# Optimization experiments

Hardware: AMD Instinct MI355X
Metric: run time of the kernel (lower is better)

## Reference

```python
import jax, jax.numpy as jnp
import numpy as np
from jax import lax

K = 3
STRIDE = 1
PAD = 1


def setup_inputs() -> dict:
    key = jax.random.key(0)
    k0, k1, k2, k3 = jax.random.split(key, 4)
    B, C, H, W, O = 8, 128, 64, 64, 128
    x = jax.random.normal(k0, (B, C, H, W), jnp.float32)
    # offset_conv: Conv2d(C, 2*K*K) - small init so sampled offsets stay moderate
    w_off = jax.random.normal(k1, (2 * K * K, C, K, K), jnp.float32) * 0.01
    b_off = jnp.zeros((2 * K * K,), jnp.float32)
    # deform_conv main weight, kaiming-ish scale
    w_def = jax.random.normal(k2, (O, C, K, K), jnp.float32) * (1.0 / np.sqrt(C * K * K))
    b_def = jax.random.normal(k3, (O,), jnp.float32) * 0.01
    return {"x": x, "w_off": w_off, "b_off": b_off, "w_def": w_def, "b_def": b_def}


def _conv2d(x, w, b, stride, pad):
    y = lax.conv_general_dilated(
        x, w, window_strides=(stride, stride), padding=[(pad, pad), (pad, pad)],
        dimension_numbers=("NCHW", "OIHW", "NCHW"))
    return y + b[None, :, None, None]


def _bilinear_sample(x, py, px):
    """x: [B,C,Hin,Win]; py,px: [B,KK,H,W] -> [B,C,KK,H,W] with zero padding."""
    B, C, Hin, Win = x.shape
    iy0f = jnp.floor(py)
    ix0f = jnp.floor(px)
    wy = py - iy0f  # grad of floor is 0, so d(wy)/d(py) = 1 (matches deform conv)
    wx = px - ix0f
    iy0 = iy0f.astype(jnp.int32)
    ix0 = ix0f.astype(jnp.int32)

    def gather(iy, ix):
        valid = (iy >= 0) & (iy < Hin) & (ix >= 0) & (ix < Win)
        iyc = jnp.clip(iy, 0, Hin - 1)
        ixc = jnp.clip(ix, 0, Win - 1)
        g = jax.vmap(lambda xb, a, b: xb[:, a, b])(x, iyc, ixc)  # [B,C,KK,H,W]
        return g * valid[:, None].astype(x.dtype)

    v00 = gather(iy0, ix0)
    v01 = gather(iy0, ix0 + 1)
    v10 = gather(iy0 + 1, ix0)
    v11 = gather(iy0 + 1, ix0 + 1)
    wy_ = wy[:, None]
    wx_ = wx[:, None]
    return (v00 * (1 - wy_) * (1 - wx_) + v01 * (1 - wy_) * wx_
            + v10 * wy_ * (1 - wx_) + v11 * wy_ * wx_)


def reference(x, w_off, b_off, w_def, b_def):
    B, C, H, W = x.shape
    O = w_def.shape[0]
    KK = K * K
    # 1) standard conv predicting offsets: [B, 2*KK, Hout, Wout]
    offsets = _conv2d(x, w_off, b_off, STRIDE, PAD)
    Hout, Wout = offsets.shape[2], offsets.shape[3]
    # torchvision layout: interleaved (dy, dx) per kernel tap
    off = offsets.reshape(B, KK, 2, Hout, Wout)
    off_y, off_x = off[:, :, 0], off[:, :, 1]  # [B,KK,Hout,Wout]
    # 2) base sampling grid per kernel tap
    kys, kxs = jnp.meshgrid(jnp.arange(K), jnp.arange(K), indexing="ij")
    kys = kys.reshape(KK).astype(jnp.float32)
    kxs = kxs.reshape(KK).astype(jnp.float32)
    hs = (jnp.arange(Hout) * STRIDE - PAD).astype(jnp.float32)
    ws = (jnp.arange(Wout) * STRIDE - PAD).astype(jnp.float32)
    base_y = hs[None, :, None] + kys[:, None, None]  # [KK,Hout,1]
    base_x = ws[None, None, :] + kxs[:, None, None]  # [KK,1,Wout]
    py = base_y[None] + off_y  # [B,KK,Hout,Wout]
    px = base_x[None] + off_x
    # 3) gather bilinear-sampled patches then dense contraction (im2col GEMM)
    sampled = _bilinear_sample(x, py, px)  # [B,C,KK,Hout,Wout]
    out = jnp.einsum("bckhw,ock->bohw", sampled, w_def.reshape(O, C, KK))
    return out + b_def[None, :, None, None]
```

## Files before the change

kernel.cpp:

```cpp
#include <hip/hip_runtime.h>
#include <hip/hip_bf16.h>

#define BB 8
#define CC 128
#define HH 64
#define WW 64
#define OO 128
#define NJ 18
#define HW 4096

typedef unsigned short u16;
typedef unsigned int u32;
typedef __attribute__((ext_vector_type(8))) __bf16 bf16x8;
typedef __attribute__((ext_vector_type(4))) float f32x4;

__device__ __forceinline__ u16 f2bf(float f) {
    u32 u = __float_as_uint(f);
    u += 0x7fffu + ((u >> 16) & 1u);
    return (u16)(u >> 16);
}
__device__ __forceinline__ float bflo(u32 u) { return __uint_as_float(u << 16); }
__device__ __forceinline__ float bfhi(u32 u) { return __uint_as_float(u & 0xffff0000u); }
__device__ __forceinline__ u32 pk2bf(float s0, float s1) {
    union { __hip_bfloat162 h; u32 u; } cv;
    cv.h = __float22bfloat162_rn(make_float2(s0, s1));
    return cv.u;
}

__global__ __launch_bounds__(256)
void k_xT(const float* __restrict__ x, u16* __restrict__ xT) {
    __shared__ float tile[64][129];
    const int t = threadIdx.x;
    const int b = blockIdx.x >> 6;
    const int hw0 = (blockIdx.x & 63) << 6;
    const float* xb = x + (size_t)b * CC * HW + hw0;
    const int tw = t & 63, tc = t >> 6;
#pragma unroll
    for (int r = 0; r < 32; ++r) {
        int c = r * 4 + tc;
        tile[tw][c] = xb[c * HW + tw];
    }
    __syncthreads();
    u16* dst = xT + ((size_t)b * HW + hw0) * CC;
#pragma unroll
    for (int r = 0; r < 4; ++r) {
        int item = t + (r << 8);
        int seg = item & 15, hw = item >> 4;
        union { u32 d[4]; uint4 v; } p;
#pragma unroll
        for (int i = 0; i < 4; ++i)
            p.d[i] = pk2bf(tile[hw][seg * 8 + 2 * i], tile[hw][seg * 8 + 2 * i + 1]);
        *(uint4*)&dst[hw * CC + seg * 8] = p.v;
    }
}

__global__ void k_prep(const float* __restrict__ w_def,
                       const float* __restrict__ w_off,
                       u16* __restrict__ wT, u16* __restrict__ wA) {
    int idx = blockIdx.x * 256 + threadIdx.x;
    if (idx < 9 * OO * CC) {
        int c = idx & 127, o = (idx >> 7) & 127, kk = idx >> 14;
        wT[idx] = f2bf(w_def[(o * CC + c) * 9 + kk]);
    }
    if (idx < 32 * 1152) {
        int k = idx % 1152, j = idx / 1152;
        int q = k >> 7, c = k & 127;
        wA[idx] = (j < NJ) ? f2bf(w_off[(j * CC + c) * 9 + q]) : (u16)0;
    }
}

__global__ __launch_bounds__(256, 2)
void k_off(const u16* __restrict__ xT, const u16* __restrict__ wA,
           const float* __restrict__ b_off, float* __restrict__ offs) {
    __shared__ u16 s_x[198 * 128];
    const int t = threadIdx.x, lane = t & 63, wv = t >> 6;
    const int posl = lane & 15, kg = lane >> 4;
    const int b = blockIdx.x & 7, h = blockIdx.x >> 3;

    for (int it = t; it < 3168; it += 256) {
        int seg = it & 15, pix = it >> 4;
        int r = pix / 66, wp = pix - r * 66;
        int y = h - 1 + r, w = wp - 1;
        uint4 v = make_uint4(0, 0, 0, 0);
        if (y >= 0 && y < HH && w >= 0 && w < WW)
            v = *(const uint4*)&xT[((size_t)(b * HW) + y * WW + w) * CC + seg * 8];
        *(uint4*)&s_x[pix * 128 + ((seg ^ (pix & 15)) * 8)] = v;
    }
    __syncthreads();

    f32x4 acc0 = {0.f, 0.f, 0.f, 0.f}, acc1 = {0.f, 0.f, 0.f, 0.f};
    for (int q = 0; q < 9; ++q) {
        int qy = q / 3, qx = q - qy * 3;
        int pix = qy * 66 + (wv * 16 + posl) + qx;
        int prow = pix * 128, pxor = pix & 15;
#pragma unroll
        for (int ki = 0; ki < 4; ++ki) {
            int ks = q * 4 + ki;
            int cidx = ki * 4 + kg;
            bf16x8 bfr = *(const bf16x8*)&s_x[prow + ((cidx ^ pxor) * 8)];
            bf16x8 a0 = *(const bf16x8*)&wA[posl * 1152 + ks * 32 + kg * 8];
            bf16x8 a1 = *(const bf16x8*)&wA[(16 + posl) * 1152 + ks * 32 + kg * 8];
            acc0 = __builtin_amdgcn_mfma_f32_16x16x32_bf16(a0, bfr, acc0, 0, 0, 0);
            acc1 = __builtin_amdgcn_mfma_f32_16x16x32_bf16(a1, bfr, acc1, 0, 0, 0);
        }
    }
    const int pos = wv * 16 + posl;
#pragma unroll
    for (int r = 0; r < 4; ++r) {
        int j = kg * 4 + r;
        offs[(b * NJ + j) * HW + h * WW + pos] = acc0[r] + b_off[j];
    }
#pragma unroll
    for (int r = 0; r < 4; ++r) {
        int j = 16 + kg * 4 + r;
        if (j < NJ) offs[(b * NJ + j) * HW + h * WW + pos] = acc1[r] + b_off[j];
    }
}

__global__ __launch_bounds__(256, 2)
void k_main(const u16* __restrict__ xT, const float* __restrict__ offs,
            const u16* __restrict__ wT, const float* __restrict__ b_def,
            float* __restrict__ out) {
    __shared__ u16 s_samp[64 * 128];

    const int t = threadIdx.x, lane = t & 63, wv = t >> 6;
    const int posl = lane & 15, kg = lane >> 4;
    const int b = blockIdx.x & 7;
    const int h = blockIdx.x >> 3;
    const char* xb = (const char*)xT + (size_t)b * (HW * CC * 2);

    const int gpos = t >> 2;
    const int segsub = t & 3;

    f32x4 acc[4][2];
#pragma unroll
    for (int mt = 0; mt < 4; ++mt) {
        acc[mt][0] = (f32x4){0.f, 0.f, 0.f, 0.f};
        acc[mt][1] = (f32x4){0.f, 0.f, 0.f, 0.f};
    }

#pragma unroll 1
    for (int kk = 0; kk < 9; ++kk) {
        int ky = kk / 3, kx = kk - ky * 3;
        float oy = offs[(b * NJ + 2 * kk) * HW + h * WW + gpos];
        float ox = offs[(b * NJ + 2 * kk + 1) * HW + h * WW + gpos];
        float py = (float)(h - 1 + ky) + oy;
        float px = (float)(gpos - 1 + kx) + ox;
        float fy = floorf(py), fx = floorf(px);
        int iy0 = (int)fy, ix0 = (int)fx;
        float wy = py - fy, wx = px - fx;
        int iy1 = iy0 + 1, ix1 = ix0 + 1;
        float my0 = (iy0 >= 0 && iy0 < HH) ? 1.0f : 0.0f;
        float my1 = (iy1 >= 0 && iy1 < HH) ? 1.0f : 0.0f;
        float mx0 = (ix0 >= 0 && ix0 < WW) ? 1.0f : 0.0f;
        float mx1 = (ix1 >= 0 && ix1 < WW) ? 1.0f : 0.0f;
        int iy0c = min(max(iy0, 0), HH - 1), iy1c = min(max(iy1, 0), HH - 1);
        int ix0c = min(max(ix0, 0), WW - 1), ix1c = min(max(ix1, 0), WW - 1);
        float wy1 = 1.0f - wy, wx1 = 1.0f - wx;
        float cwx = my0 * mx0 * wy1 * wx1, cwy = my0 * mx1 * wy1 * wx;
        float cwz = my1 * mx0 * wy * wx1,  cww = my1 * mx1 * wy * wx;
        int cox = (iy0c * WW + ix0c) << 8, coy = (iy0c * WW + ix1c) << 8;
        int coz = (iy1c * WW + ix0c) << 8, cow = (iy1c * WW + ix1c) << 8;

        const int slotbase = gpos * 128;
        const int pxor = gpos & 15;
#pragma unroll
        for (int j = 0; j < 4; ++j) {
            const int seg = segsub + 4 * j;
            const int sb = seg * 16;
            uint4 q00 = *(const uint4*)(xb + cox + sb);
            uint4 q01 = *(const uint4*)(xb + coy + sb);
            uint4 q10 = *(const uint4*)(xb + coz + sb);
            uint4 q11 = *(const uint4*)(xb + cow + sb);
            const u32* u00 = (const u32*)&q00;
            const u32* u01 = (const u32*)&q01;
            const u32* u10 = (const u32*)&q10;
            const u32* u11 = (const u32*)&q11;
            union { u32 d[4]; uint4 v; } p;
#pragma unroll
            for (int i = 0; i < 4; ++i) {
                float s0 = cwx * bflo(u00[i]) + cwy * bflo(u01[i])
                         + cwz * bflo(u10[i]) + cww * bflo(u11[i]);
                float s1 = cwx * bfhi(u00[i]) + cwy * bfhi(u01[i])
                         + cwz * bfhi(u10[i]) + cww * bfhi(u11[i]);
                p.d[i] = pk2bf(s0, s1);
            }
            *(uint4*)&s_samp[slotbase + ((seg ^ pxor) * 8)] = p.v;
        }
        __syncthreads();

        {
            const int o0 = wv * 32;
            const u16* wkk = wT + kk * (OO * CC);
            bf16x8 wfr[4][2];
#pragma unroll
            for (int ct = 0; ct < 4; ++ct) {
#pragma unroll
                for (int nt = 0; nt < 2; ++nt) {
                    int o = o0 + nt * 16 + posl;
                    wfr[ct][nt] = *(const bf16x8*)&wkk[o * CC + ct * 32 + kg * 8];
                }
            }
#pragma unroll
            for (int ct = 0; ct < 4; ++ct) {
                const int chunk = ct * 4 + kg;
#pragma unroll
                for (int mt = 0; mt < 4; ++mt) {
                    bf16x8 afr = *(const bf16x8*)
                        &s_samp[(mt * 16 + posl) * 128 + ((chunk ^ posl) * 8)];
                    acc[mt][0] = __builtin_amdgcn_mfma_f32_16x16x32_bf16(
                        afr, wfr[ct][0], acc[mt][0], 0, 0, 0);
                    acc[mt][1] = __builtin_amdgcn_mfma_f32_16x16x32_bf16(
                        afr, wfr[ct][1], acc[mt][1], 0, 0, 0);
                }
            }
        }
        __syncthreads();
    }

#pragma unroll
    for (int nt = 0; nt < 2; ++nt) {
        const int o = wv * 32 + nt * 16 + posl;
        const float bd = b_def[o];
        float* orow = out + ((b * OO + o) * HH + h) * WW;
#pragma unroll
        for (int mt = 0; mt < 4; ++mt) {
            float4 res;
            res.x = acc[mt][nt][0] + bd;
            res.y = acc[mt][nt][1] + bd;
            res.z = acc[mt][nt][2] + bd;
            res.w = acc[mt][nt][3] + bd;
            *(float4*)&orow[mt * 16 + kg * 4] = res;
        }
    }
}

extern "C" void kernel_launch(void* const* d_in, const int* in_sizes, int n_in,
                              void* d_out, int out_size, void* d_ws, size_t ws_size,
                              hipStream_t stream) {
    const float* x     = (const float*)d_in[0];
    const float* w_off = (const float*)d_in[1];
    const float* b_off = (const float*)d_in[2];
    const float* w_def = (const float*)d_in[3];
    const float* b_def = (const float*)d_in[4];
    float* out = (float*)d_out;

    float* offs = (float*)d_ws;
    u16*   xT   = (u16*)(offs + BB * NJ * HW);
    u16*   wT   = xT + (size_t)BB * HW * CC;
    u16*   wA   = wT + 9 * OO * CC;

    k_xT  <<<512, 256, 0, stream>>>(x, xT);
    k_prep<<<576, 256, 0, stream>>>(w_def, w_off, wT, wA);
    k_off <<<512, 256, 0, stream>>>(xT, wA, b_off, offs);
    k_main<<<512, 256, 0, stream>>>(xT, offs, wT, b_def, out);
}
```

Measured before the change: 139.5 us.

## Double-buffer sampled tile and prefetch next tap's gather during MFMA

Splits the shared sample buffer into two halves and software-pipelines the kernel-tap loop. The next tap's offsets and bilinear gather loads are issued before the current tap's MFMA work, then interpolated into the alternate buffer afterwards, which drops one barrier per iteration. The goal is to hide global gather latency behind the matrix math. In exchange it holds 16 uint4 registers of prefetched data across the MFMA section and doubles LDS use to 32KB, which may lower occupancy under launch_bounds(256,2) or cause spills.

```diff
diff --git a/kernel.cpp b/kernel.cpp
--- a/kernel.cpp
+++ b/kernel.cpp
@@ -121,7 +121,7 @@
 void k_main(const u16* __restrict__ xT, const float* __restrict__ offs,
             const u16* __restrict__ wT, const float* __restrict__ b_def,
             float* __restrict__ out) {
-    __shared__ u16 s_samp[64 * 128];
+    __shared__ u16 s_samp[2][64 * 128];
 
     const int t = threadIdx.x, lane = t & 63, wv = t >> 6;
     const int posl = lane & 15, kg = lane >> 4;
@@ -131,16 +131,10 @@
 
     const int gpos = t >> 2;
     const int segsub = t & 3;
-
-    f32x4 acc[4][2];
-#pragma unroll
-    for (int mt = 0; mt < 4; ++mt) {
-        acc[mt][0] = (f32x4){0.f, 0.f, 0.f, 0.f};
-        acc[mt][1] = (f32x4){0.f, 0.f, 0.f, 0.f};
-    }
-
-#pragma unroll 1
-    for (int kk = 0; kk < 9; ++kk) {
+    const int pxor = gpos & 15;
+    const int slotbase = gpos * 128;
+
+    auto coords = [&](int kk, float4& cw, int4& co) {
         int ky = kk / 3, kx = kk - ky * 3;
         float oy = offs[(b * NJ + 2 * kk) * HW + h * WW + gpos];
         float ox = offs[(b * NJ + 2 * kk + 1) * HW + h * WW + gpos];
@@ -157,37 +151,65 @@
         int iy0c = min(max(iy0, 0), HH - 1), iy1c = min(max(iy1, 0), HH - 1);
         int ix0c = min(max(ix0, 0), WW - 1), ix1c = min(max(ix1, 0), WW - 1);
         float wy1 = 1.0f - wy, wx1 = 1.0f - wx;
-        float cwx = my0 * mx0 * wy1 * wx1, cwy = my0 * mx1 * wy1 * wx;
-        float cwz = my1 * mx0 * wy * wx1,  cww = my1 * mx1 * wy * wx;
-        int cox = (iy0c * WW + ix0c) << 8, coy = (iy0c * WW + ix1c) << 8;
-        int coz = (iy1c * WW + ix0c) << 8, cow = (iy1c * WW + ix1c) << 8;
-
-        const int slotbase = gpos * 128;
-        const int pxor = gpos & 15;
+        cw = make_float4(my0 * mx0 * wy1 * wx1, my0 * mx1 * wy1 * wx,
+                         my1 * mx0 * wy  * wx1, my1 * mx1 * wy  * wx);
+        co = make_int4((iy0c * WW + ix0c) << 8, (iy0c * WW + ix1c) << 8,
+                       (iy1c * WW + ix0c) << 8, (iy1c * WW + ix1c) << 8);
+    };
+    auto issue_gather = [&](const int4 co, uint4 q[4][4]) {
+#pragma unroll
+        for (int j = 0; j < 4; ++j) {
+            const int sb = (segsub + 4 * j) * 16;
+            q[j][0] = *(const uint4*)(xb + co.x + sb);
+            q[j][1] = *(const uint4*)(xb + co.y + sb);
+            q[j][2] = *(const uint4*)(xb + co.z + sb);
+            q[j][3] = *(const uint4*)(xb + co.w + sb);
+        }
+    };
+    auto interp_store = [&](const float4 cw, uint4 q[4][4], int p) {
 #pragma unroll
         for (int j = 0; j < 4; ++j) {
             const int seg = segsub + 4 * j;
-            const int sb = seg * 16;
-            uint4 q00 = *(const uint4*)(xb + cox + sb);
-            uint4 q01 = *(const uint4*)(xb + coy + sb);
-            uint4 q10 = *(const uint4*)(xb + coz + sb);
-            uint4 q11 = *(const uint4*)(xb + cow + sb);
-            const u32* u00 = (const u32*)&q00;
-            const u32* u01 = (const u32*)&q01;
-            const u32* u10 = (const u32*)&q10;
-            const u32* u11 = (const u32*)&q11;
-            union { u32 d[4]; uint4 v; } p;
+            const u32* u00 = (const u32*)&q[j][0];
+            const u32* u01 = (const u32*)&q[j][1];
+            const u32* u10 = (const u32*)&q[j][2];
+            const u32* u11 = (const u32*)&q[j][3];
+            union { u32 d[4]; uint4 v; } pk;
 #pragma unroll
             for (int i = 0; i < 4; ++i) {
-                float s0 = cwx * bflo(u00[i]) + cwy * bflo(u01[i])
-                         + cwz * bflo(u10[i]) + cww * bflo(u11[i]);
-                float s1 = cwx * bfhi(u00[i]) + cwy * bfhi(u01[i])
-                         + cwz * bfhi(u10[i]) + cww * bfhi(u11[i]);
-                p.d[i] = pk2bf(s0, s1);
+                float s0 = cw.x * bflo(u00[i]) + cw.y * bflo(u01[i])
+                         + cw.z * bflo(u10[i]) + cw.w * bflo(u11[i]);
+                float s1 = cw.x * bfhi(u00[i]) + cw.y * bfhi(u01[i])
+                         + cw.z * bfhi(u10[i]) + cw.w * bfhi(u11[i]);
+                pk.d[i] = pk2bf(s0, s1);
             }
-            *(uint4*)&s_samp[slotbase + ((seg ^ pxor) * 8)] = p.v;
-        }
-        __syncthreads();
+            *(uint4*)&s_samp[p][slotbase + ((seg ^ pxor) * 8)] = pk.v;
+        }
+    };
+
+    f32x4 acc[4][2];
+#pragma unroll
+    for (int mt = 0; mt < 4; ++mt) {
+        acc[mt][0] = (f32x4){0.f, 0.f, 0.f, 0.f};
+        acc[mt][1] = (f32x4){0.f, 0.f, 0.f, 0.f};
+    }
+
+    float4 cw; int4 co;
+    uint4 q[4][4];
+    coords(0, cw, co);
+    issue_gather(co, q);
+    interp_store(cw, q, 0);
+    __syncthreads();
+
+#pragma unroll 1
+    for (int kk = 0; kk < 9; ++kk) {
+        const int p = kk & 1;
+
+        float4 cwN; int4 coN;
+        if (kk < 8) {
+            coords(kk + 1, cwN, coN);
+            issue_gather(coN, q);
+        }
 
         {
             const int o0 = wv * 32;
@@ -207,7 +229,7 @@
 #pragma unroll
                 for (int mt = 0; mt < 4; ++mt) {
                     bf16x8 afr = *(const bf16x8*)
-                        &s_samp[(mt * 16 + posl) * 128 + ((chunk ^ posl) * 8)];
+                        &s_samp[p][(mt * 16 + posl) * 128 + ((chunk ^ posl) * 8)];
                     acc[mt][0] = __builtin_amdgcn_mfma_f32_16x16x32_bf16(
                         afr, wfr[ct][0], acc[mt][0], 0, 0, 0);
                     acc[mt][1] = __builtin_amdgcn_mfma_f32_16x16x32_bf16(
@@ -215,7 +237,11 @@
                 }
             }
         }
-        __syncthreads();
+
+        if (kk < 8) {
+            interp_store(cwN, q, p ^ 1);
+            __syncthreads();
+        }
     }
 
 #pragma unroll
```

Result: faster. 133.8 us (-4.1%).
